# Optimization experiments

Hardware: AMD Instinct MI355X
Metric: run time of the kernel (lower is better)

Reference implementation:

```python
import jax, jax.numpy as jnp
import numpy as np

B, N, T, FD = 128, 64, 20, 2
E, H, A = 16, 32, 32
DB, DH = 30.0, 30.0
NB, NHD = 12, 12  # 360/30 bearing and heading bins
DOMAIN_INIT = 5.0
EPS = 1e-12


def setup_inputs() -> dict:
    key = jax.random.key(0)
    ks = jax.random.split(key, 20)
    rn = lambda k, s, sc=0.1: (jax.random.normal(k, s) * sc).astype(jnp.float32)
    return {
        'x': jax.random.normal(ks[0], (B, N, T, FD), jnp.float32),
        'dmat': jax.random.uniform(ks[1], (B, N, T, N), jnp.float32) * 10.0,
        'bmat': jax.random.uniform(ks[2], (B, N, T, N), jnp.float32) * 360.0,
        'hmat': jax.random.uniform(ks[3], (B, N, T, N), jnp.float32) * 360.0,
        'mask': jnp.ones((B, N, T), jnp.float32),
        'emb_W': rn(ks[4], (E, FD)), 'emb_b': rn(ks[5], (E,)),
        'W_ih': rn(ks[6], (4 * H, E)), 'W_hh': rn(ks[7], (4 * H, H)),
        'b_ih': rn(ks[8], (4 * H,)), 'b_hh': rn(ks[9], (4 * H,)),
        'domain': jnp.full((NB, NHD), DOMAIN_INIT, jnp.float32),
        'enc2att_W': rn(ks[10], (A, H)), 'enc2att_b': rn(ks[11], (A,)),
        'spa_W': rn(ks[12], (A, 2 * A)), 'spa_b': rn(ks[13], (A,)),
        'att2enc_W': rn(ks[14], (H, A)), 'att2enc_b': rn(ks[15], (H,)),
        'cls_W': rn(ks[16], (1, H)), 'cls_b': rn(ks[17], (1,)),
        'h0': jax.random.normal(ks[18], (B * N, H), jnp.float32),
        'c0': jax.random.normal(ks[19], (B * N, H), jnp.float32),
    }


def _forward(x, dmat, bmat, hmat, mask, emb_W, emb_b, W_ih, W_hh, b_ih, b_hh,
             domain, enc2att_W, enc2att_b, spa_W, spa_b, att2enc_W, att2enc_b,
             cls_W, cls_b, h0, c0):
    # input embedding: [B,N,T,F] -> [T, B*N, E] (time-major for scan)
    xe = jnp.einsum('bntf,ef->bnte', x, emb_W) + emb_b
    xe = jnp.moveaxis(xe.reshape(B * N, T, E), 1, 0)
    dm_t = jnp.moveaxis(dmat, 2, 0)   # [T,B,N,N]
    bm_t = jnp.moveaxis(bmat, 2, 0)
    hm_t = jnp.moveaxis(hmat, 2, 0)
    mk_t = jnp.moveaxis(mask, 2, 0)   # [T,B,N]
    eye = jnp.eye(N, dtype=x.dtype)

    def step(carry, inputs):
        h, c = carry                     # [B*N, H]
        xt, dm, bm, hm, mk = inputs
        # single-step LSTM cell (torch gate order i,f,g,o)
        g = xt @ W_ih.T + b_ih + h @ W_hh.T + b_hh
        i, f, gg, o = jnp.split(g, 4, axis=-1)
        c = jax.nn.sigmoid(f) * c + jax.nn.sigmoid(i) * jnp.tanh(gg)
        h = jax.nn.sigmoid(o) * jnp.tanh(c)
        # project encoder state to attention space: [B,N,A]
        a = h.reshape(B, N, H) @ enc2att_W.T + enc2att_b
        # spatial attention weights from distance/bearing/heading edge feats
        ib = jnp.clip(jnp.floor(bm / DB), 0, NB - 1).astype(jnp.int32)
        ih = jnp.clip(jnp.floor(hm / DH), 0, NHD - 1).astype(jnp.int32)
        w = jax.nn.relu(domain[ib, ih] - dm)               # [B,N,N]
        w = w * mk[:, :, None] * mk[:, None, :] * (1.0 - eye)
        w = w / (jnp.sum(w, axis=-1, keepdims=True) + EPS)
        att = jnp.einsum('bij,bjd->bid', w, a)
        z = jnp.tanh(jnp.concatenate([a, att], axis=-1) @ spa_W.T + spa_b)
        h = (z @ att2enc_W.T + att2enc_b).reshape(B * N, H)
        return (h, c), None

    (h, c), _ = jax.lax.scan(step, (h0, c0), (xe, dm_t, bm_t, hm_t, mk_t))
    scores = jnp.tanh(h.reshape(B, N, H) @ cls_W.T + cls_b)
    return jax.nn.sigmoid(scores)  # [B, N, 1]


def reference(x, dmat, bmat, hmat, mask, emb_W, emb_b, W_ih, W_hh, b_ih, b_hh,
              domain, enc2att_W, enc2att_b, spa_W, spa_b, att2enc_W, att2enc_b,
              cls_W, cls_b, h0, c0):
    return _forward(x, dmat, bmat, hmat, mask, emb_W, emb_b, W_ih, W_hh, b_ih,
                    b_hh, domain, enc2att_W, enc2att_b, spa_W, spa_b,
                    att2enc_W, att2enc_b, cls_W, cls_b, h0, c0)
```

## Files before the change

kernel.cpp:

```cpp
#include <hip/hip_runtime.h>
#include <math.h>

#define T_STEPS 20

typedef _Float16 half8 __attribute__((ext_vector_type(8)));
typedef _Float16 half4v __attribute__((ext_vector_type(4)));
typedef float f32x4 __attribute__((ext_vector_type(4)));

__device__ __forceinline__ float sigm(float v) {
  return __builtin_amdgcn_rcpf(1.0f + __expf(-v));
}
__device__ __forceinline__ float tanh_f(float v) {
  return 1.0f - 2.0f * __builtin_amdgcn_rcpf(1.0f + __expf(2.0f * v));
}

__device__ __forceinline__ void barrier_lgkm() {
  asm volatile("s_waitcnt lgkmcnt(0)" ::: "memory");
  __builtin_amdgcn_s_barrier();
  asm volatile("" ::: "memory");
}

__global__ __launch_bounds__(1024)
void traj_disc(const float* __restrict__ x, const float* __restrict__ dmat,
               const float* __restrict__ bmat, const float* __restrict__ hmat,
               const float* __restrict__ maskp,
               const float* __restrict__ embW, const float* __restrict__ embb,
               const float* __restrict__ Wih, const float* __restrict__ Whh,
               const float* __restrict__ bih, const float* __restrict__ bhh,
               const float* __restrict__ dom,
               const float* __restrict__ e2aW, const float* __restrict__ e2ab,
               const float* __restrict__ spaW, const float* __restrict__ spab,
               const float* __restrict__ a2eW, const float* __restrict__ a2eb,
               const float* __restrict__ clsW, const float* __restrict__ clsb,
               const float* __restrict__ h0p, const float* __restrict__ c0p,
               float* __restrict__ out)
{
  __shared__ __align__(16) _Float16 sgw[128*40];
  __shared__ __align__(16) _Float16 sgwc[128*40];
  __shared__ __align__(16) float4   sgmb[128];
  __shared__ __align__(16) _Float16 sESaT[32*40];
  __shared__ __align__(16) _Float16 sEStT[32*40];
  __shared__ float bz[32];
  __shared__ float sdom[144];
  __shared__ float sm[1280];
  __shared__ float sclsc[32];
  __shared__ float sclsb2[1];
  __shared__ __align__(16) _Float16 sH[64*40];
  __shared__ __align__(16) _Float16 sw[64*72];
  __shared__ __align__(16) _Float16 sz_[64*40];
  __shared__ __align__(16) _Float16 sQT[32*72];

  const int tid = threadIdx.x;
  const int b = blockIdx.x;
  const int w = tid >> 6;
  const int l = tid & 63;
  const int quad = l >> 4;
  const int n16 = l & 15;

  for (int idx = tid; idx < 4096; idx += 1024) sgw[(idx >> 5)*40 + (idx & 31)] = (_Float16)Whh[idx];
  {
    const int g = tid >> 3, kb = (tid & 7) << 2;
    float a0 = 0.f, a1 = 0.f, a2 = 0.f, a3 = 0.f;
    #pragma unroll
    for (int h = 0; h < 32; ++h) {
      const float wv = Whh[g*32 + h];
      a0 = fmaf(wv, a2eW[h*32 + kb + 0], a0);
      a1 = fmaf(wv, a2eW[h*32 + kb + 1], a1);
      a2 = fmaf(wv, a2eW[h*32 + kb + 2], a2);
      a3 = fmaf(wv, a2eW[h*32 + kb + 3], a3);
    }
    sgwc[g*40 + kb + 0] = (_Float16)a0; sgwc[g*40 + kb + 1] = (_Float16)a1;
    sgwc[g*40 + kb + 2] = (_Float16)a2; sgwc[g*40 + kb + 3] = (_Float16)a3;
  }
  if (tid < 128) {
    float m0 = 0.f, m1 = 0.f, b0 = bih[tid] + bhh[tid];
    #pragma unroll
    for (int e = 0; e < 16; ++e) {
      float wv_ = Wih[tid*16 + e];
      m0 = fmaf(wv_, embW[2*e],   m0);
      m1 = fmaf(wv_, embW[2*e+1], m1);
      b0 = fmaf(wv_, embb[e],     b0);
    }
    float bn = b0;
    #pragma unroll
    for (int h = 0; h < 32; ++h) bn = fmaf(Whh[tid*32 + h], a2eb[h], bn);
    sgmb[tid] = make_float4(m0, m1, b0, bn);
  }
  {
    const int zk = tid >> 5, hc = tid & 31;
    float sa_ = 0.f, st_ = 0.f;
    #pragma unroll
    for (int a = 0; a < 32; ++a) {
      const float ev = e2aW[a*32 + hc];
      sa_ = fmaf(spaW[zk*64 + a],      ev, sa_);
      st_ = fmaf(spaW[zk*64 + 32 + a], ev, st_);
    }
    sESaT[zk*40 + hc] = (_Float16)sa_;
    sEStT[zk*40 + hc] = (_Float16)st_;
  }
  if (tid < 32) {
    float acc = spab[tid];
    #pragma unroll
    for (int a = 0; a < 32; ++a)
      acc = fmaf(e2ab[a], spaW[tid*64 + a] + spaW[tid*64 + 32 + a], acc);
    bz[tid] = acc;
    float cc = 0.f;
    #pragma unroll
    for (int h = 0; h < 32; ++h) cc = fmaf(clsW[h], a2eW[h*32 + tid], cc);
    sclsc[tid] = cc;
  }
  if (tid == 0) {
    float cb = clsb[0];
    #pragma unroll
    for (int h = 0; h < 32; ++h) cb = fmaf(clsW[h], a2eb[h], cb);
    sclsb2[0] = cb;
  }
  if (tid < 144) sdom[tid] = dom[tid];
  for (int idx = tid; idx < 1280; idx += 1024) sm[idx] = maskp[(size_t)b*1280 + idx];
  for (int idx = tid; idx < 2048; idx += 1024) sz_[(idx >> 5)*40 + (idx & 31)] = (_Float16)h0p[(size_t)b*2048 + idx];

  f32x4 ccell;
  float2 xA, xB, xC, xD;
  f32x4 dmv0, dmv1, bmv0, bmv1, hmv0, hmv1;
  const float* xpre = nullptr;
  size_t ebp = 0;
  if (w < 8) {
    const int rr = w >> 1, uu = w & 1;
    const int hh = 16*uu + n16;
    #pragma unroll
    for (int reg = 0; reg < 4; ++reg)
      ccell[reg] = c0p[(size_t)b*2048 + (size_t)(16*rr + 4*quad + reg)*32 + hh];
    xpre = x + (size_t)(b*64 + 16*rr + 4*quad) * 40;
    xA = *(const float2*)(xpre +   0);
    xB = *(const float2*)(xpre +  40);
    xC = *(const float2*)(xpre +  80);
    xD = *(const float2*)(xpre + 120);
  } else {
    const int i8 = (tid - 512) >> 3, s8 = tid & 7;
    ebp = ((size_t)(b*64 + i8)*20)*64 + (size_t)(s8*8);
    dmv0 = *(const f32x4*)(dmat + ebp); dmv1 = *(const f32x4*)(dmat + ebp + 4);
    bmv0 = *(const f32x4*)(bmat + ebp); bmv1 = *(const f32x4*)(bmat + ebp + 4);
    hmv0 = *(const f32x4*)(hmat + ebp); hmv1 = *(const f32x4*)(hmat + ebp + 4);
  }
  __syncthreads();

  #pragma unroll 1
  for (int t = 0; t < T_STEPS; ++t) {
    if (w < 8) {
      const int rr = w >> 1, uu = w & 1;
      const _Float16* Bbase = (t == 0) ? sgw : sgwc;
      const half8 Af = *(const half8*)(sz_ + (16*rr + n16)*40 + quad*8);
      f32x4 G0, G1, G2, G3;
#define OP1Q(Gq, q) { \
      const int c_ = 2*(q) + uu; \
      const half8 Bf = *(const half8*)(Bbase + (16*c_ + n16)*40 + quad*8); \
      const float4 mb = sgmb[16*c_ + n16]; \
      const float bb = (t == 0) ? mb.z : mb.w; \
      f32x4 Cv; \
      Cv[0] = fmaf(xA.x, mb.x, fmaf(xA.y, mb.y, bb)); \
      Cv[1] = fmaf(xB.x, mb.x, fmaf(xB.y, mb.y, bb)); \
      Cv[2] = fmaf(xC.x, mb.x, fmaf(xC.y, mb.y, bb)); \
      Cv[3] = fmaf(xD.x, mb.x, fmaf(xD.y, mb.y, bb)); \
      Gq = __builtin_amdgcn_mfma_f32_16x16x32_f16(Af, Bf, Cv, 0, 0, 0); }
      OP1Q(G0, 0) OP1Q(G1, 1) OP1Q(G2, 2) OP1Q(G3, 3)
#undef OP1Q
      const int hh = 16*uu + n16;
      #pragma unroll
      for (int reg = 0; reg < 4; ++reg) {
        const float cc = fmaf(sigm(G1[reg]), ccell[reg], sigm(G0[reg]) * tanh_f(G2[reg]));
        ccell[reg] = cc;
        sH[(16*rr + 4*quad + reg)*40 + hh] = (_Float16)(sigm(G3[reg]) * tanh_f(cc));
      }
      const int tn2 = ((t < T_STEPS - 1) ? t + 1 : t) << 1;
      xA = *(const float2*)(xpre + tn2);
      xB = *(const float2*)(xpre + tn2 +  40);
      xC = *(const float2*)(xpre + tn2 +  80);
      xD = *(const float2*)(xpre + tn2 + 120);
    } else {
      const int i8 = (tid - 512) >> 3, s8 = tid & 7;
      const float mi_ = sm[i8*20 + t];
      f32x4 wnA, wnB;
      float rs = 0.0f;
#define WC(dst, k, dmv, bmv, hmv, jof) { \
      int ib_ = (int)floorf(bmv[k] * (1.0f/30.0f)); ib_ = ib_ < 0 ? 0 : (ib_ > 11 ? 11 : ib_); \
      int ih_ = (int)floorf(hmv[k] * (1.0f/30.0f)); ih_ = ih_ < 0 ? 0 : (ih_ > 11 ? 11 : ih_); \
      float w_ = fmaxf(sdom[ib_*12 + ih_] - dmv[k], 0.0f) * (mi_ * sm[(8*s8 + (jof))*20 + t]); \
      w_ = (8*s8 + (jof) == i8) ? 0.0f : w_; dst[k] = w_; rs += w_; }
      WC(wnA,0,dmv0,bmv0,hmv0,0) WC(wnA,1,dmv0,bmv0,hmv0,1)
      WC(wnA,2,dmv0,bmv0,hmv0,2) WC(wnA,3,dmv0,bmv0,hmv0,3)
      WC(wnB,0,dmv1,bmv1,hmv1,4) WC(wnB,1,dmv1,bmv1,hmv1,5)
      WC(wnB,2,dmv1,bmv1,hmv1,6) WC(wnB,3,dmv1,bmv1,hmv1,7)
#undef WC
      rs += __shfl_xor(rs, 1); rs += __shfl_xor(rs, 2); rs += __shfl_xor(rs, 4);
      const float inv_ = __builtin_amdgcn_rcpf(rs + 1e-12f);
      half8 hw;
      hw[0] = (_Float16)(wnA[0]*inv_); hw[1] = (_Float16)(wnA[1]*inv_);
      hw[2] = (_Float16)(wnA[2]*inv_); hw[3] = (_Float16)(wnA[3]*inv_);
      hw[4] = (_Float16)(wnB[0]*inv_); hw[5] = (_Float16)(wnB[1]*inv_);
      hw[6] = (_Float16)(wnB[2]*inv_); hw[7] = (_Float16)(wnB[3]*inv_);
      *(half8*)(sw + i8*72 + s8*8) = hw;
      const int tn = (t < T_STEPS - 1) ? t + 1 : t;
      const size_t eb2 = ebp + (size_t)tn*64;
      dmv0 = *(const f32x4*)(dmat + eb2); dmv1 = *(const f32x4*)(dmat + eb2 + 4);
      bmv0 = *(const f32x4*)(bmat + eb2); bmv1 = *(const f32x4*)(bmat + eb2 + 4);
      hmv0 = *(const f32x4*)(hmat + eb2); hmv1 = *(const f32x4*)(hmat + eb2 + 4);
    }
    barrier_lgkm();

    f32x4 Pv = {0.f, 0.f, 0.f, 0.f};
    if (w < 8) {
      const int r = w >> 1, c = w & 1;
      const half8 Af = *(const half8*)(sH    + (16*r + n16)*40 + quad*8);
      const half8 Bf = *(const half8*)(sESaT + (16*c + n16)*40 + quad*8);
      const float bzv = bz[16*c + n16];
      Pv[0] = bzv; Pv[1] = bzv; Pv[2] = bzv; Pv[3] = bzv;
      Pv = __builtin_amdgcn_mfma_f32_16x16x32_f16(Af, Bf, Pv, 0, 0, 0);
    } else {
      const int w8 = w - 8, r = w8 >> 1, c = w8 & 1;
      const half8 Af = *(const half8*)(sH    + (16*r + n16)*40 + quad*8);
      const half8 Bf = *(const half8*)(sEStT + (16*c + n16)*40 + quad*8);
      f32x4 Cv = {0.f, 0.f, 0.f, 0.f};
      Cv = __builtin_amdgcn_mfma_f32_16x16x32_f16(Af, Bf, Cv, 0, 0, 0);
      half4v hq;
      hq[0] = (_Float16)Cv[0]; hq[1] = (_Float16)Cv[1];
      hq[2] = (_Float16)Cv[2]; hq[3] = (_Float16)Cv[3];
      *(half4v*)(sQT + (16*c + n16)*72 + 16*r + 4*quad) = hq;
    }
    barrier_lgkm();

    if (w < 8) {
      const int r = w >> 1, c = w & 1;
      const half8 A0 = *(const half8*)(sw  + (16*r + n16)*72 + quad*8);
      const half8 A1 = *(const half8*)(sw  + (16*r + n16)*72 + 32 + quad*8);
      const half8 B0 = *(const half8*)(sQT + (16*c + n16)*72 + quad*8);
      const half8 B1 = *(const half8*)(sQT + (16*c + n16)*72 + 32 + quad*8);
      Pv = __builtin_amdgcn_mfma_f32_16x16x32_f16(A0, B0, Pv, 0, 0, 0);
      Pv = __builtin_amdgcn_mfma_f32_16x16x32_f16(A1, B1, Pv, 0, 0, 0);
      const int nd = 16*r + 4*quad;
      sz_[(nd+0)*40 + 16*c + n16] = (_Float16)tanh_f(Pv[0]);
      sz_[(nd+1)*40 + 16*c + n16] = (_Float16)tanh_f(Pv[1]);
      sz_[(nd+2)*40 + 16*c + n16] = (_Float16)tanh_f(Pv[2]);
      sz_[(nd+3)*40 + 16*c + n16] = (_Float16)tanh_f(Pv[3]);
    }
    barrier_lgkm();
  }

  if (tid < 64) {
    float acc = sclsb2[0];
    #pragma unroll
    for (int k = 0; k < 32; ++k) acc = fmaf((float)sz_[tid*40 + k], sclsc[k], acc);
    out[(size_t)b*64 + tid] = sigm(tanh_f(acc));
  }
}

extern "C" void kernel_launch(void* const* d_in, const int* in_sizes, int n_in,
                              void* d_out, int out_size, void* d_ws, size_t ws_size,
                              hipStream_t stream) {
  (void)in_sizes; (void)n_in; (void)d_ws; (void)ws_size; (void)out_size;
  const float* x    = (const float*)d_in[0];
  const float* dmat = (const float*)d_in[1];
  const float* bmat = (const float*)d_in[2];
  const float* hmat = (const float*)d_in[3];
  const float* mask = (const float*)d_in[4];
  const float* embW = (const float*)d_in[5];
  const float* embb = (const float*)d_in[6];
  const float* Wih  = (const float*)d_in[7];
  const float* Whh  = (const float*)d_in[8];
  const float* bih  = (const float*)d_in[9];
  const float* bhh  = (const float*)d_in[10];
  const float* dom  = (const float*)d_in[11];
  const float* e2aW = (const float*)d_in[12];
  const float* e2ab = (const float*)d_in[13];
  const float* spaW = (const float*)d_in[14];
  const float* spab = (const float*)d_in[15];
  const float* a2eW = (const float*)d_in[16];
  const float* a2eb = (const float*)d_in[17];
  const float* clsW = (const float*)d_in[18];
  const float* clsb = (const float*)d_in[19];
  const float* h0   = (const float*)d_in[20];
  const float* c0   = (const float*)d_in[21];
  float* out = (float*)d_out;

  traj_disc<<<dim3(128), dim3(1024), 0, stream>>>(
      x, dmat, bmat, hmat, mask, embW, embb, Wih, Whh, bih, bhh, dom,
      e2aW, e2ab, spaW, spab, a2eW, a2eb, clsW, clsb, h0, c0, out);
}
```

Before: 206.4 us.

## Pipeline spatial weights one step ahead and remove a per-step barrier

The edge-weight computation is moved one timestep ahead into a double-buffered shared array, so it runs concurrently with the LSTM phase of the previous step. The Q=H·EStT product is now computed redundantly by each LSTM wave into a private scratch buffer, which removes one block-wide barrier per step and the cross-wave hand-off. The mask is also transposed in shared memory so per-step reads are contiguous. In exchange each wave does four extra MFMAs per step and shared memory use grows, and the LSTM waves now carry the whole attention workload serially.

```diff
diff --git a/kernel.cpp b/kernel.cpp
--- a/kernel.cpp
+++ b/kernel.cpp
@@ -4,7 +4,7 @@
 #define T_STEPS 20
 
 typedef _Float16 half8 __attribute__((ext_vector_type(8)));
-typedef _Float16 half4v __attribute__((ext_vector_type(4)));
+typedef __fp16 fp16x2 __attribute__((ext_vector_type(2)));
 typedef float f32x4 __attribute__((ext_vector_type(4)));
 
 __device__ __forceinline__ float sigm(float v) {
@@ -18,6 +18,15 @@
   asm volatile("s_waitcnt lgkmcnt(0)" ::: "memory");
   __builtin_amdgcn_s_barrier();
   asm volatile("" ::: "memory");
+}
+
+__device__ __forceinline__ int2 pkpair(const f32x4 D) {
+  const fp16x2 p0 = __builtin_amdgcn_cvt_pkrtz(D[0], D[1]);
+  const fp16x2 p1 = __builtin_amdgcn_cvt_pkrtz(D[2], D[3]);
+  int2 r;
+  r.x = __builtin_bit_cast(int, p0);
+  r.y = __builtin_bit_cast(int, p1);
+  return r;
 }
 
 __global__ __launch_bounds__(1024)
@@ -46,9 +55,10 @@
   __shared__ float sclsc[32];
   __shared__ float sclsb2[1];
   __shared__ __align__(16) _Float16 sH[64*40];
-  __shared__ __align__(16) _Float16 sw[64*72];
+  __shared__ __align__(16) _Float16 swA[64*72];
+  __shared__ __align__(16) _Float16 swB[64*72];
   __shared__ __align__(16) _Float16 sz_[64*40];
-  __shared__ __align__(16) _Float16 sQT[32*72];
+  __shared__ __align__(16) _Float16 sqb[8*16*72];
 
   const int tid = threadIdx.x;
   const int b = blockIdx.x;
@@ -56,6 +66,8 @@
   const int l = tid & 63;
   const int quad = l >> 4;
   const int n16 = l & 15;
+  const int i8 = (tid >= 512) ? ((tid - 512) >> 3) : 0;
+  const int s8 = tid & 7;
 
   for (int idx = tid; idx < 4096; idx += 1024) sgw[(idx >> 5)*40 + (idx & 31)] = (_Float16)Whh[idx];
   {
@@ -116,7 +128,8 @@
     sclsb2[0] = cb;
   }
   if (tid < 144) sdom[tid] = dom[tid];
-  for (int idx = tid; idx < 1280; idx += 1024) sm[idx] = maskp[(size_t)b*1280 + idx];
+  for (int idx = tid; idx < 1280; idx += 1024)
+    sm[idx] = maskp[(size_t)b*1280 + (size_t)(idx & 63)*20 + (idx >> 6)];
   for (int idx = tid; idx < 2048; idx += 1024) sz_[(idx >> 5)*40 + (idx & 31)] = (_Float16)h0p[(size_t)b*2048 + idx];
 
   f32x4 ccell;
@@ -124,19 +137,18 @@
   f32x4 dmv0, dmv1, bmv0, bmv1, hmv0, hmv1;
   const float* xpre = nullptr;
   size_t ebp = 0;
+  const int r = w >> 1, c = w & 1;
   if (w < 8) {
-    const int rr = w >> 1, uu = w & 1;
-    const int hh = 16*uu + n16;
+    const int hh = 16*c + n16;
     #pragma unroll
     for (int reg = 0; reg < 4; ++reg)
-      ccell[reg] = c0p[(size_t)b*2048 + (size_t)(16*rr + 4*quad + reg)*32 + hh];
-    xpre = x + (size_t)(b*64 + 16*rr + 4*quad) * 40;
+      ccell[reg] = c0p[(size_t)b*2048 + (size_t)(16*r + 4*quad + reg)*32 + hh];
+    xpre = x + (size_t)(b*64 + 16*r + 4*quad) * 40;
     xA = *(const float2*)(xpre +   0);
     xB = *(const float2*)(xpre +  40);
     xC = *(const float2*)(xpre +  80);
     xD = *(const float2*)(xpre + 120);
   } else {
-    const int i8 = (tid - 512) >> 3, s8 = tid & 7;
     ebp = ((size_t)(b*64 + i8)*20)*64 + (size_t)(s8*8);
     dmv0 = *(const f32x4*)(dmat + ebp); dmv1 = *(const f32x4*)(dmat + ebp + 4);
     bmv0 = *(const f32x4*)(bmat + ebp); bmv1 = *(const f32x4*)(bmat + ebp + 4);
@@ -144,15 +156,51 @@
   }
   __syncthreads();
 
+#define WC(dst, k, dmv, bmv, hmv, jof) { \
+  int ib_ = (int)floorf(bmv[k] * (1.0f/30.0f)); ib_ = ib_ < 0 ? 0 : (ib_ > 11 ? 11 : ib_); \
+  int ih_ = (int)floorf(hmv[k] * (1.0f/30.0f)); ih_ = ih_ < 0 ? 0 : (ih_ > 11 ? 11 : ih_); \
+  float w_ = fmaxf(sdom[ib_*12 + ih_] - dmv[k], 0.0f) * (mi_ * sm[tloc*64 + 8*s8 + (jof)]); \
+  w_ = (8*s8 + (jof) == i8) ? 0.0f : w_; dst[k] = w_; rs += w_; }
+
+#define DO_3A(tn_, swdst) { \
+  const int tloc = (tn_); \
+  const float mi_ = sm[tloc*64 + i8]; \
+  f32x4 wnA, wnB; float rs = 0.0f; \
+  WC(wnA,0,dmv0,bmv0,hmv0,0) WC(wnA,1,dmv0,bmv0,hmv0,1) \
+  WC(wnA,2,dmv0,bmv0,hmv0,2) WC(wnA,3,dmv0,bmv0,hmv0,3) \
+  WC(wnB,0,dmv1,bmv1,hmv1,4) WC(wnB,1,dmv1,bmv1,hmv1,5) \
+  WC(wnB,2,dmv1,bmv1,hmv1,6) WC(wnB,3,dmv1,bmv1,hmv1,7) \
+  rs += __shfl_xor(rs, 1); rs += __shfl_xor(rs, 2); rs += __shfl_xor(rs, 4); \
+  const float inv_ = __builtin_amdgcn_rcpf(rs + 1e-12f); \
+  half8 hw; \
+  hw[0] = (_Float16)(wnA[0]*inv_); hw[1] = (_Float16)(wnA[1]*inv_); \
+  hw[2] = (_Float16)(wnA[2]*inv_); hw[3] = (_Float16)(wnA[3]*inv_); \
+  hw[4] = (_Float16)(wnB[0]*inv_); hw[5] = (_Float16)(wnB[1]*inv_); \
+  hw[6] = (_Float16)(wnB[2]*inv_); hw[7] = (_Float16)(wnB[3]*inv_); \
+  *(half8*)((swdst) + i8*72 + s8*8) = hw; }
+
+  half8 EStB{}, ESaB{};
+  float bzv = 0.f;
+  if (w < 8) {
+    EStB = *(const half8*)(sEStT + (16*c + n16)*40 + quad*8);
+    ESaB = *(const half8*)(sESaT + (16*c + n16)*40 + quad*8);
+    bzv = bz[16*c + n16];
+  } else {
+    DO_3A(0, swA);
+    const size_t eb1 = ebp + 64;
+    dmv0 = *(const f32x4*)(dmat + eb1); dmv1 = *(const f32x4*)(dmat + eb1 + 4);
+    bmv0 = *(const f32x4*)(bmat + eb1); bmv1 = *(const f32x4*)(bmat + eb1 + 4);
+    hmv0 = *(const f32x4*)(hmat + eb1); hmv1 = *(const f32x4*)(hmat + eb1 + 4);
+  }
+
   #pragma unroll 1
   for (int t = 0; t < T_STEPS; ++t) {
     if (w < 8) {
-      const int rr = w >> 1, uu = w & 1;
       const _Float16* Bbase = (t == 0) ? sgw : sgwc;
-      const half8 Af = *(const half8*)(sz_ + (16*rr + n16)*40 + quad*8);
+      const half8 Af = *(const half8*)(sz_ + (16*r + n16)*40 + quad*8);
       f32x4 G0, G1, G2, G3;
 #define OP1Q(Gq, q) { \
-      const int c_ = 2*(q) + uu; \
+      const int c_ = 2*(q) + c; \
       const half8 Bf = *(const half8*)(Bbase + (16*c_ + n16)*40 + quad*8); \
       const float4 mb = sgmb[16*c_ + n16]; \
       const float bb = (t == 0) ? mb.z : mb.w; \
@@ -164,12 +212,12 @@
       Gq = __builtin_amdgcn_mfma_f32_16x16x32_f16(Af, Bf, Cv, 0, 0, 0); }
       OP1Q(G0, 0) OP1Q(G1, 1) OP1Q(G2, 2) OP1Q(G3, 3)
 #undef OP1Q
-      const int hh = 16*uu + n16;
+      const int hh = 16*c + n16;
       #pragma unroll
       for (int reg = 0; reg < 4; ++reg) {
         const float cc = fmaf(sigm(G1[reg]), ccell[reg], sigm(G0[reg]) * tanh_f(G2[reg]));
         ccell[reg] = cc;
-        sH[(16*rr + 4*quad + reg)*40 + hh] = (_Float16)(sigm(G3[reg]) * tanh_f(cc));
+        sH[(16*r + 4*quad + reg)*40 + hh] = (_Float16)(sigm(G3[reg]) * tanh_f(cc));
       }
       const int tn2 = ((t < T_STEPS - 1) ? t + 1 : t) << 1;
       xA = *(const float2*)(xpre + tn2);
@@ -177,65 +225,42 @@
       xC = *(const float2*)(xpre + tn2 +  80);
       xD = *(const float2*)(xpre + tn2 + 120);
     } else {
-      const int i8 = (tid - 512) >> 3, s8 = tid & 7;
-      const float mi_ = sm[i8*20 + t];
-      f32x4 wnA, wnB;
-      float rs = 0.0f;
-#define WC(dst, k, dmv, bmv, hmv, jof) { \
-      int ib_ = (int)floorf(bmv[k] * (1.0f/30.0f)); ib_ = ib_ < 0 ? 0 : (ib_ > 11 ? 11 : ib_); \
-      int ih_ = (int)floorf(hmv[k] * (1.0f/30.0f)); ih_ = ih_ < 0 ? 0 : (ih_ > 11 ? 11 : ih_); \
-      float w_ = fmaxf(sdom[ib_*12 + ih_] - dmv[k], 0.0f) * (mi_ * sm[(8*s8 + (jof))*20 + t]); \
-      w_ = (8*s8 + (jof) == i8) ? 0.0f : w_; dst[k] = w_; rs += w_; }
-      WC(wnA,0,dmv0,bmv0,hmv0,0) WC(wnA,1,dmv0,bmv0,hmv0,1)
-      WC(wnA,2,dmv0,bmv0,hmv0,2) WC(wnA,3,dmv0,bmv0,hmv0,3)
-      WC(wnB,0,dmv1,bmv1,hmv1,4) WC(wnB,1,dmv1,bmv1,hmv1,5)
-      WC(wnB,2,dmv1,bmv1,hmv1,6) WC(wnB,3,dmv1,bmv1,hmv1,7)
-#undef WC
-      rs += __shfl_xor(rs, 1); rs += __shfl_xor(rs, 2); rs += __shfl_xor(rs, 4);
-      const float inv_ = __builtin_amdgcn_rcpf(rs + 1e-12f);
-      half8 hw;
-      hw[0] = (_Float16)(wnA[0]*inv_); hw[1] = (_Float16)(wnA[1]*inv_);
-      hw[2] = (_Float16)(wnA[2]*inv_); hw[3] = (_Float16)(wnA[3]*inv_);
-      hw[4] = (_Float16)(wnB[0]*inv_); hw[5] = (_Float16)(wnB[1]*inv_);
-      hw[6] = (_Float16)(wnB[2]*inv_); hw[7] = (_Float16)(wnB[3]*inv_);
-      *(half8*)(sw + i8*72 + s8*8) = hw;
       const int tn = (t < T_STEPS - 1) ? t + 1 : t;
-      const size_t eb2 = ebp + (size_t)tn*64;
+      _Float16* swn = ((t + 1) & 1) ? swB : swA;
+      DO_3A(tn, swn);
+      const int tp = (t < T_STEPS - 2) ? t + 2 : T_STEPS - 1;
+      const size_t eb2 = ebp + (size_t)tp*64;
       dmv0 = *(const f32x4*)(dmat + eb2); dmv1 = *(const f32x4*)(dmat + eb2 + 4);
       bmv0 = *(const f32x4*)(bmat + eb2); bmv1 = *(const f32x4*)(bmat + eb2 + 4);
       hmv0 = *(const f32x4*)(hmat + eb2); hmv1 = *(const f32x4*)(hmat + eb2 + 4);
     }
     barrier_lgkm();
 
-    f32x4 Pv = {0.f, 0.f, 0.f, 0.f};
     if (w < 8) {
-      const int r = w >> 1, c = w & 1;
-      const half8 Af = *(const half8*)(sH    + (16*r + n16)*40 + quad*8);
-      const half8 Bf = *(const half8*)(sESaT + (16*c + n16)*40 + quad*8);
-      const float bzv = bz[16*c + n16];
-      Pv[0] = bzv; Pv[1] = bzv; Pv[2] = bzv; Pv[3] = bzv;
-      Pv = __builtin_amdgcn_mfma_f32_16x16x32_f16(Af, Bf, Pv, 0, 0, 0);
-    } else {
-      const int w8 = w - 8, r = w8 >> 1, c = w8 & 1;
-      const half8 Af = *(const half8*)(sH    + (16*r + n16)*40 + quad*8);
-      const half8 Bf = *(const half8*)(sEStT + (16*c + n16)*40 + quad*8);
-      f32x4 Cv = {0.f, 0.f, 0.f, 0.f};
-      Cv = __builtin_amdgcn_mfma_f32_16x16x32_f16(Af, Bf, Cv, 0, 0, 0);
-      half4v hq;
-      hq[0] = (_Float16)Cv[0]; hq[1] = (_Float16)Cv[1];
-      hq[2] = (_Float16)Cv[2]; hq[3] = (_Float16)Cv[3];
-      *(half4v*)(sQT + (16*c + n16)*72 + 16*r + 4*quad) = hq;
-    }
-    barrier_lgkm();
-
-    if (w < 8) {
-      const int r = w >> 1, c = w & 1;
-      const half8 A0 = *(const half8*)(sw  + (16*r + n16)*72 + quad*8);
-      const half8 A1 = *(const half8*)(sw  + (16*r + n16)*72 + 32 + quad*8);
-      const half8 B0 = *(const half8*)(sQT + (16*c + n16)*72 + quad*8);
-      const half8 B1 = *(const half8*)(sQT + (16*c + n16)*72 + 32 + quad*8);
-      Pv = __builtin_amdgcn_mfma_f32_16x16x32_f16(A0, B0, Pv, 0, 0, 0);
-      Pv = __builtin_amdgcn_mfma_f32_16x16x32_f16(A1, B1, Pv, 0, 0, 0);
+      const _Float16* swr = (t & 1) ? swB : swA;
+      _Float16* qb = sqb + w*(16*72);
+      const half8 a0 = *(const half8*)(sH + (     n16)*40 + quad*8);
+      const half8 a1 = *(const half8*)(sH + (16 + n16)*40 + quad*8);
+      const half8 a2 = *(const half8*)(sH + (32 + n16)*40 + quad*8);
+      const half8 a3 = *(const half8*)(sH + (48 + n16)*40 + quad*8);
+      const half8 aP = *(const half8*)(sH + (16*r + n16)*40 + quad*8);
+      const half8 A0 = *(const half8*)(swr + (16*r + n16)*72 + quad*8);
+      const half8 A1 = *(const half8*)(swr + (16*r + n16)*72 + 32 + quad*8);
+      f32x4 Pv; Pv[0] = bzv; Pv[1] = bzv; Pv[2] = bzv; Pv[3] = bzv;
+      Pv = __builtin_amdgcn_mfma_f32_16x16x32_f16(aP, ESaB, Pv, 0, 0, 0);
+      const f32x4 Z4 = {0.f, 0.f, 0.f, 0.f};
+      const f32x4 D0 = __builtin_amdgcn_mfma_f32_16x16x32_f16(a0, EStB, Z4, 0, 0, 0);
+      const f32x4 D1 = __builtin_amdgcn_mfma_f32_16x16x32_f16(a1, EStB, Z4, 0, 0, 0);
+      const f32x4 D2 = __builtin_amdgcn_mfma_f32_16x16x32_f16(a2, EStB, Z4, 0, 0, 0);
+      const f32x4 D3 = __builtin_amdgcn_mfma_f32_16x16x32_f16(a3, EStB, Z4, 0, 0, 0);
+      *(int2*)(qb + n16*72 +  0 + 4*quad) = pkpair(D0);
+      *(int2*)(qb + n16*72 + 16 + 4*quad) = pkpair(D1);
+      *(int2*)(qb + n16*72 + 32 + 4*quad) = pkpair(D2);
+      *(int2*)(qb + n16*72 + 48 + 4*quad) = pkpair(D3);
+      const half8 Bf0 = *(const half8*)(qb + n16*72 + 8*quad);
+      const half8 Bf1 = *(const half8*)(qb + n16*72 + 32 + 8*quad);
+      Pv = __builtin_amdgcn_mfma_f32_16x16x32_f16(A0, Bf0, Pv, 0, 0, 0);
+      Pv = __builtin_amdgcn_mfma_f32_16x16x32_f16(A1, Bf1, Pv, 0, 0, 0);
       const int nd = 16*r + 4*quad;
       sz_[(nd+0)*40 + 16*c + n16] = (_Float16)tanh_f(Pv[0]);
       sz_[(nd+1)*40 + 16*c + n16] = (_Float16)tanh_f(Pv[1]);
@@ -244,6 +269,9 @@
     }
     barrier_lgkm();
   }
+
+#undef DO_3A
+#undef WC
 
   if (tid < 64) {
     float acc = sclsb2[0];
```

After: 209.3 us. About the same (+1.4%).
